# Performance work log

Hardware: AMD Instinct MI355X
Metric: run time of the kernel (lower is better)

The kernel has to match this reference:

```python
import jax, jax.numpy as jnp
import numpy as np

N = 100_000   # nodes
E = 1_600_000 # edges
IN, HID, OUT = 128, 64, 32


def _glorot(key, fan_in, fan_out):
    s = jnp.sqrt(6.0 / (fan_in + fan_out)).astype(jnp.float32)
    return jax.random.uniform(key, (fan_in, fan_out), jnp.float32, -s, s)


def setup_inputs() -> dict:
    key = jax.random.key(0)
    ks = jax.random.split(key, 8)
    x = jax.random.normal(ks[0], (N, IN), jnp.float32)
    edge_index = jax.random.randint(ks[1], (2, E), 0, N, jnp.int64)
    return {
        "x": x,
        "edge_index": edge_index,
        "W1": _glorot(ks[2], IN, HID),
        "b1": jnp.zeros((HID,), jnp.float32),
        "W_mu": _glorot(ks[3], HID, OUT),
        "b_mu": jnp.zeros((OUT,), jnp.float32),
        "W_ls": _glorot(ks[4], HID, OUT),
        "b_ls": jnp.zeros((OUT,), jnp.float32),
    }


def _gcn_conv(x, W, b, src, dst, n, dinv_sqrt):
    """PyG GCNConv: h = x @ W; symmetric-normalized scatter-add incl. self-loops; + b."""
    h = x @ W                                       # [N, F_out]
    coef = dinv_sqrt[src] * dinv_sqrt[dst]          # [E]
    msg = h[src] * coef[:, None]                    # [E, F_out] gather
    agg = jax.ops.segment_sum(msg, dst, num_segments=n)  # scatter-add
    agg = agg + h * (dinv_sqrt * dinv_sqrt)[:, None]      # self-loop contribution
    return agg + b


def reference(x, edge_index, W1, b1, W_mu, b_mu, W_ls, b_ls):
    src, dst = edge_index[0], edge_index[1]
    n = x.shape[0]
    # degree on graph with self-loops (edge weight 1), shared by all three convs
    deg = jax.ops.segment_sum(jnp.ones((src.shape[0],), x.dtype), dst, num_segments=n) + 1.0
    dinv_sqrt = jax.lax.rsqrt(deg)
    h = jax.nn.relu(_gcn_conv(x, W1, b1, src, dst, n, dinv_sqrt))
    mu = _gcn_conv(h, W_mu, b_mu, src, dst, n, dinv_sqrt)
    logstd = _gcn_conv(h, W_ls, b_ls, src, dst, n, dinv_sqrt)
    return mu, logstd
```

## Files before the change

### kernel.cpp

```cpp
#include <hip/hip_runtime.h>
#include <hip/hip_bf16.h>

#define FIN 128
#define HID 64
#define BSN 128
#define BSHIFT 7
#define SRCBITS 20
#define EPB 8192
#define BSTRIDE 2304
#define STARTBITS 21

typedef __attribute__((ext_vector_type(8))) short short8;
typedef __attribute__((ext_vector_type(4))) float floatx4;

__device__ __forceinline__ float bf2f(unsigned short u) {
    union { unsigned int i; float f; } c;
    c.i = ((unsigned int)u) << 16;
    return c.f;
}

__device__ __forceinline__ unsigned short f2bf(float f) {
    union { float f; unsigned int i; } c;
    c.f = f;
    unsigned int u = c.i;
    unsigned int r = (u + 0x7FFFu + ((u >> 16) & 1u)) >> 16;
    return (unsigned short)r;
}

__global__ void bin_fill(const int* __restrict__ src, const int* __restrict__ dst,
                         int* __restrict__ bcur, unsigned* __restrict__ rec, int E) {
    __shared__ int hist[1024];
    __shared__ int cbase[1024];
    for (int i = threadIdx.x; i < 1024; i += 256) hist[i] = 0;
    __syncthreads();
    int base = blockIdx.x * EPB;
    int lim = min(base + EPB, E);
    for (int e = base + threadIdx.x; e < lim; e += 256)
        atomicAdd(&hist[dst[e] >> BSHIFT], 1);
    __syncthreads();
    for (int b = threadIdx.x; b < 1024; b += 256) {
        int c = hist[b];
        cbase[b] = c ? atomicAdd(&bcur[b], c) : 0;
    }
    __syncthreads();
    for (int i = threadIdx.x; i < 1024; i += 256) hist[i] = 0;
    __syncthreads();
    for (int e = base + threadIdx.x; e < lim; e += 256) {
        int d = dst[e];
        int bkt = d >> BSHIFT;
        int slot = atomicAdd(&hist[bkt], 1);
        rec[bkt * BSTRIDE + cbase[bkt] + slot] =
            (unsigned)src[e] | ((unsigned)(d & (BSN - 1)) << SRCBITS);
    }
}

__global__ void csr_build(const unsigned* __restrict__ rec, const int* __restrict__ bcur,
                          unsigned* __restrict__ rowp, int* __restrict__ csr, int N) {
    __shared__ int cnt[BSN], excl[BSN], cur[BSN];
    int b = blockIdx.x, t = threadIdx.x;
    if (t < BSN) cnt[t] = 0;
    __syncthreads();
    int base = b * BSTRIDE;
    int cb = bcur[b];
    for (int i = t; i < cb; i += 256)
        atomicAdd(&cnt[rec[base + i] >> SRCBITS], 1);
    __syncthreads();
    if (t < BSN) excl[t] = cnt[t];
    __syncthreads();
    for (int off = 1; off < BSN; off <<= 1) {
        int a = 0;
        if (t < BSN && t >= off) a = excl[t - off];
        __syncthreads();
        if (t < BSN) excl[t] += a;
        __syncthreads();
    }
    if (t < BSN) {
        int inc = excl[t];
        int ex = inc - cnt[t];
        excl[t] = ex;
        cur[t] = 0;
        int n = b * BSN + t;
        if (n < N)
            rowp[n] = (unsigned)(base + ex) | ((unsigned)cnt[t] << STARTBITS);
    }
    __syncthreads();
    for (int i = t; i < cb; i += 256) {
        unsigned r = rec[base + i];
        int dl = r >> SRCBITS;
        int slot = atomicAdd(&cur[dl], 1);
        csr[base + excl[dl] + slot] = (int)(r & ((1u << SRCBITS) - 1));
    }
}

__global__ __launch_bounds__(256) void gemm1_mfma(
    const float* __restrict__ x, const float* __restrict__ W1,
    const unsigned* __restrict__ rowp, unsigned short* __restrict__ h0, int N) {
    __shared__ unsigned short Wt[64][136];
    {
        int t = threadIdx.x;
        int k  = t >> 1;
        int c0 = (t & 1) << 5;
        const float* wr = W1 + k * HID + c0;
#pragma unroll
        for (int cc = 0; cc < 32; ++cc)
            Wt[c0 + cc][k] = f2bf(wr[cc]);
    }
    __syncthreads();
    int wave = threadIdx.x >> 6, lane = threadIdx.x & 63;
    int m = lane & 15, q = lane >> 4;
    short8 bfr[4][4];
#pragma unroll
    for (int ct = 0; ct < 4; ++ct)
#pragma unroll
        for (int kk = 0; kk < 4; ++kk)
            bfr[ct][kk] = *((const short8*)&Wt[ct * 16 + m][kk * 32 + q * 8]);
    int ntiles = N >> 4;
    for (int t = blockIdx.x * 4 + wave; t < ntiles; t += gridDim.x * 4) {
        int nbase = t << 4;
        const float* xr = x + (size_t)(nbase + m) * FIN + q * 8;
        short8 afr[4];
#pragma unroll
        for (int kk = 0; kk < 4; ++kk) {
            float4 p0 = *((const float4*)(xr + kk * 32));
            float4 p1 = *((const float4*)(xr + kk * 32 + 4));
            short8 ta;
            ta[0] = (short)f2bf(p0.x); ta[1] = (short)f2bf(p0.y);
            ta[2] = (short)f2bf(p0.z); ta[3] = (short)f2bf(p0.w);
            ta[4] = (short)f2bf(p1.x); ta[5] = (short)f2bf(p1.y);
            ta[6] = (short)f2bf(p1.z); ta[7] = (short)f2bf(p1.w);
            afr[kk] = ta;
        }
        uint4 rp = *((const uint4*)(rowp + nbase + q * 4));
        floatx4 cacc[4];
#pragma unroll
        for (int ct = 0; ct < 4; ++ct) cacc[ct] = floatx4{0.f, 0.f, 0.f, 0.f};
#pragma unroll
        for (int ct = 0; ct < 4; ++ct)
#pragma unroll
            for (int kk = 0; kk < 4; ++kk)
                cacc[ct] = __builtin_amdgcn_mfma_f32_16x16x32_bf16(afr[kk], bfr[ct][kk], cacc[ct], 0, 0, 0);
#pragma unroll
        for (int ct = 0; ct < 4; ++ct) {
#pragma unroll
            for (int r = 0; r < 4; ++r) {
                unsigned pr = (r == 0) ? rp.x : (r == 1) ? rp.y : (r == 2) ? rp.z : rp.w;
                float d = rsqrtf((float)(pr >> STARTBITS) + 1.0f);
                int n = nbase + q * 4 + r;
                h0[(size_t)n * HID + ct * 16 + m] = f2bf(cacc[ct][r] * d);
            }
        }
    }
}


#define ACC8(a, d)                                                      \
    do {                                                                \
        union { unsigned u; float f; } c_;                              \
        c_.u = (d).x << 16;          a[0] += c_.f;                      \
        c_.u = (d).x & 0xFFFF0000u;  a[1] += c_.f;                      \
        c_.u = (d).y << 16;          a[2] += c_.f;                      \
        c_.u = (d).y & 0xFFFF0000u;  a[3] += c_.f;                      \
        c_.u = (d).z << 16;          a[4] += c_.f;                      \
        c_.u = (d).z & 0xFFFF0000u;  a[5] += c_.f;                      \
        c_.u = (d).w << 16;          a[6] += c_.f;                      \
        c_.u = (d).w & 0xFFFF0000u;  a[7] += c_.f;                      \
    } while (0)

template <int MODE>
__global__ __launch_bounds__(256, 4) void pull(
    const unsigned short* __restrict__ hp,
    const unsigned* __restrict__ rowp,
    const int* __restrict__ csr,
    const float* __restrict__ b1,
    unsigned short* __restrict__ outp,
    const float* __restrict__ Wmu, const float* __restrict__ bmu,
    const float* __restrict__ Wls, const float* __restrict__ bls,
    float* __restrict__ out, int N) {
    int lane = threadIdx.x & 63;
    int wave = threadIdx.x >> 6;
    int nd8  = lane >> 3;
    int g    = lane & 7;
    int n = blockIdx.x * 32 + wave * 8 + nd8;
    bool valid = (n < N);
    int nc = valid ? n : 0;
    unsigned rp = rowp[nc];
    int start = (int)(rp & ((1u << STARTBITS) - 1u));
    int deg   = (int)(rp >> STARTBITS);
    int end   = valid ? start + deg : 0;
    if (!valid) start = 0;
    const char* hpb = (const char*)hp;
    unsigned goff = (unsigned)(g << 4);
    uint4 sv = *((const uint4*)(hpb + (((unsigned)nc) << 7) + goff));
    float di = rsqrtf((float)deg + 1.0f);
    float4 bb0 = *((const float4*)(b1 + (g << 3)));
    float4 bb1 = *((const float4*)(b1 + (g << 3) + 4));
    float a[8] = {0.f, 0.f, 0.f, 0.f, 0.f, 0.f, 0.f, 0.f};
    int j = start;
    for (; j + 8 <= end; j += 8) {
        int s0 = csr[j],     s1 = csr[j + 1], s2 = csr[j + 2], s3 = csr[j + 3];
        int s4 = csr[j + 4], s5 = csr[j + 5], s6 = csr[j + 6], s7 = csr[j + 7];
        uint4 d0 = *((const uint4*)(hpb + (((unsigned)s0) << 7) + goff));
        uint4 d1 = *((const uint4*)(hpb + (((unsigned)s1) << 7) + goff));
        uint4 d2 = *((const uint4*)(hpb + (((unsigned)s2) << 7) + goff));
        uint4 d3 = *((const uint4*)(hpb + (((unsigned)s3) << 7) + goff));
        uint4 d4 = *((const uint4*)(hpb + (((unsigned)s4) << 7) + goff));
        uint4 d5 = *((const uint4*)(hpb + (((unsigned)s5) << 7) + goff));
        uint4 d6 = *((const uint4*)(hpb + (((unsigned)s6) << 7) + goff));
        uint4 d7 = *((const uint4*)(hpb + (((unsigned)s7) << 7) + goff));
        ACC8(a, d0); ACC8(a, d1); ACC8(a, d2); ACC8(a, d3);
        ACC8(a, d4); ACC8(a, d5); ACC8(a, d6); ACC8(a, d7);
    }
    if (j + 4 <= end) {
        int s0 = csr[j], s1 = csr[j + 1], s2 = csr[j + 2], s3 = csr[j + 3];
        uint4 d0 = *((const uint4*)(hpb + (((unsigned)s0) << 7) + goff));
        uint4 d1 = *((const uint4*)(hpb + (((unsigned)s1) << 7) + goff));
        uint4 d2 = *((const uint4*)(hpb + (((unsigned)s2) << 7) + goff));
        uint4 d3 = *((const uint4*)(hpb + (((unsigned)s3) << 7) + goff));
        ACC8(a, d0); ACC8(a, d1); ACC8(a, d2); ACC8(a, d3);
        j += 4;
    }
    if (j < end) {
        int i0 = j, i1 = min(j + 1, end - 1), i2 = min(j + 2, end - 1);
        int s0 = csr[i0], s1 = csr[i1], s2 = csr[i2];
        uint4 d0 = *((const uint4*)(hpb + (((unsigned)s0) << 7) + goff));
        uint4 d1 = *((const uint4*)(hpb + (((unsigned)s1) << 7) + goff));
        uint4 d2 = *((const uint4*)(hpb + (((unsigned)s2) << 7) + goff));
        if (j + 1 >= end) { d1.x = 0u; d1.y = 0u; d1.z = 0u; d1.w = 0u; }
        if (j + 2 >= end) { d2.x = 0u; d2.y = 0u; d2.z = 0u; d2.w = 0u; }
        ACC8(a, d0); ACC8(a, d1); ACC8(a, d2);
    }
    uint4 o = {0u, 0u, 0u, 0u};
    if (valid) {
        ACC8(a, sv);
        float v[8];
        if (MODE == 0) {
            float t0;
            t0 = di * a[0] + bb0.x; v[0] = (t0 > 0.f ? t0 : 0.f) * di;
            t0 = di * a[1] + bb0.y; v[1] = (t0 > 0.f ? t0 : 0.f) * di;
            t0 = di * a[2] + bb0.z; v[2] = (t0 > 0.f ? t0 : 0.f) * di;
            t0 = di * a[3] + bb0.w; v[3] = (t0 > 0.f ? t0 : 0.f) * di;
            t0 = di * a[4] + bb1.x; v[4] = (t0 > 0.f ? t0 : 0.f) * di;
            t0 = di * a[5] + bb1.y; v[5] = (t0 > 0.f ? t0 : 0.f) * di;
            t0 = di * a[6] + bb1.z; v[6] = (t0 > 0.f ? t0 : 0.f) * di;
            t0 = di * a[7] + bb1.w; v[7] = (t0 > 0.f ? t0 : 0.f) * di;
        } else {
#pragma unroll
            for (int k = 0; k < 8; ++k) v[k] = di * a[k];
        }
        o.x = (unsigned)f2bf(v[0]) | ((unsigned)f2bf(v[1]) << 16);
        o.y = (unsigned)f2bf(v[2]) | ((unsigned)f2bf(v[3]) << 16);
        o.z = (unsigned)f2bf(v[4]) | ((unsigned)f2bf(v[5]) << 16);
        o.w = (unsigned)f2bf(v[6]) | ((unsigned)f2bf(v[7]) << 16);
    }
    if constexpr (MODE == 0) {
        if (valid)
            *((uint4*)(outp + (size_t)n * HID + (g << 3))) = o;
    } else {
        __shared__ unsigned short ab[32][68];
        *((uint4*)&ab[wave * 8 + nd8][g << 3]) = o;
        __syncthreads();
        int m = lane & 15, q = lane >> 4;
        int tileId = wave >> 1;
        int ct0 = (wave & 1) * 2;
        short8 a0 = *((const short8*)&ab[tileId * 16 + m][q * 8]);
        short8 a1 = *((const short8*)&ab[tileId * 16 + m][32 + q * 8]);
        short8 bfr[2][2];
        float bias[2];
#pragma unroll
        for (int c = 0; c < 2; ++c) {
            int col = (ct0 + c) * 16 + m;
#pragma unroll
            for (int kk = 0; kk < 2; ++kk) {
                short8 tf;
#pragma unroll
                for (int jj = 0; jj < 8; ++jj) {
                    int k = kk * 32 + q * 8 + jj;
                    float w = (col < 32) ? Wmu[k * 32 + col] : Wls[k * 32 + (col - 32)];
                    tf[jj] = (short)f2bf(w);
                }
                bfr[c][kk] = tf;
            }
            bias[c] = (col < 32) ? bmu[col] : bls[col - 32];
        }
        floatx4 cc[2];
#pragma unroll
        for (int c = 0; c < 2; ++c) cc[c] = floatx4{0.f, 0.f, 0.f, 0.f};
#pragma unroll
        for (int c = 0; c < 2; ++c) {
            cc[c] = __builtin_amdgcn_mfma_f32_16x16x32_bf16(a0, bfr[c][0], cc[c], 0, 0, 0);
            cc[c] = __builtin_amdgcn_mfma_f32_16x16x32_bf16(a1, bfr[c][1], cc[c], 0, 0, 0);
        }
        int nb = blockIdx.x * 32 + tileId * 16;
#pragma unroll
        for (int c = 0; c < 2; ++c) {
            int col = (ct0 + c) * 16 + m;
            int which = col >> 5, oc = col & 31;
#pragma unroll
            for (int r = 0; r < 4; ++r) {
                int n2 = nb + q * 4 + r;
                if (n2 < N)
                    out[(size_t)which * N * 32 + (size_t)n2 * 32 + oc] = cc[c][r] + bias[c];
            }
        }
    }
}

extern "C" void kernel_launch(void* const* d_in, const int* in_sizes, int n_in,
                              void* d_out, int out_size, void* d_ws, size_t ws_size,
                              hipStream_t stream) {
    const float* x   = (const float*)d_in[0];
    const int*   ei  = (const int*)d_in[1];
    const float* W1  = (const float*)d_in[2];
    const float* b1  = (const float*)d_in[3];
    const float* Wmu = (const float*)d_in[4];
    const float* bmu = (const float*)d_in[5];
    const float* Wls = (const float*)d_in[6];
    const float* bls = (const float*)d_in[7];
    int N = in_sizes[0] / FIN;
    int E = in_sizes[1] / 2;
    const int* src = ei;
    const int* dst = ei + E;
    float* out = (float*)d_out;

    int B = (N + BSN - 1) / BSN;
    int nbin = (E + EPB - 1) / EPB;

    unsigned* rowp = (unsigned*)d_ws;
    int* bcur = (int*)(rowp + N);
    int* csr  = bcur + B;
    unsigned short* bufA = (unsigned short*)(csr + (size_t)B * BSTRIDE);
    char* region2 = (char*)(bufA + (size_t)N * HID);
    unsigned* rec        = (unsigned*)region2;
    unsigned short* bufB = (unsigned short*)region2;

    hipMemsetAsync(bcur, 0, (size_t)B * sizeof(int), stream);
    bin_fill<<<nbin, 256, 0, stream>>>(src, dst, bcur, rec, E);
    csr_build<<<B, 256, 0, stream>>>(rec, bcur, rowp, csr, N);

    gemm1_mfma<<<512, 256, 0, stream>>>(x, W1, rowp, bufA, N);

    int pgrid = (N + 31) / 32;
    pull<0><<<pgrid, 256, 0, stream>>>(bufA, rowp, csr, b1, bufB,
                                       Wmu, bmu, Wls, bls, out, N);
    pull<1><<<pgrid, 256, 0, stream>>>(bufB, rowp, csr, b1, (unsigned short*)0,
                                       Wmu, bmu, Wls, bls, out, N);
}
```

Before: 260.9 us.

## Replace shared-memory histogram binning with direct padded global atomics

The binning kernel drops its two-pass per-block shared histogram and reservation scheme. Each edge now does a global atomicAdd on a per-bucket counter, padded to 16 ints so counters sit on separate cache lines, and writes its record straight into the bucket. The grid becomes a fixed 2048-block grid-stride loop. This removes the extra pass over dst and the block barriers, at the cost of one global atomic per edge (1.6M) with contention spread over about 782 buckets.

```diff
diff --git a/kernel.cpp b/kernel.cpp
--- a/kernel.cpp
+++ b/kernel.cpp
@@ -6,9 +6,9 @@
 #define BSN 128
 #define BSHIFT 7
 #define SRCBITS 20
-#define EPB 8192
 #define BSTRIDE 2304
 #define STARTBITS 21
+#define BPAD 16
 
 typedef __attribute__((ext_vector_type(8))) short short8;
 typedef __attribute__((ext_vector_type(4))) float floatx4;
@@ -27,30 +27,18 @@
     return (unsigned short)r;
 }
 
-__global__ void bin_fill(const int* __restrict__ src, const int* __restrict__ dst,
-                         int* __restrict__ bcur, unsigned* __restrict__ rec, int E) {
-    __shared__ int hist[1024];
-    __shared__ int cbase[1024];
-    for (int i = threadIdx.x; i < 1024; i += 256) hist[i] = 0;
-    __syncthreads();
-    int base = blockIdx.x * EPB;
-    int lim = min(base + EPB, E);
-    for (int e = base + threadIdx.x; e < lim; e += 256)
-        atomicAdd(&hist[dst[e] >> BSHIFT], 1);
-    __syncthreads();
-    for (int b = threadIdx.x; b < 1024; b += 256) {
-        int c = hist[b];
-        cbase[b] = c ? atomicAdd(&bcur[b], c) : 0;
-    }
-    __syncthreads();
-    for (int i = threadIdx.x; i < 1024; i += 256) hist[i] = 0;
-    __syncthreads();
-    for (int e = base + threadIdx.x; e < lim; e += 256) {
+__global__ __launch_bounds__(256) void bin_fill(
+    const int* __restrict__ src, const int* __restrict__ dst,
+    int* __restrict__ bcur, unsigned* __restrict__ rec, int E) {
+    int i = blockIdx.x * 256 + threadIdx.x;
+    int stride = gridDim.x * 256;
+    for (int e = i; e < E; e += stride) {
         int d = dst[e];
+        int s = src[e];
         int bkt = d >> BSHIFT;
-        int slot = atomicAdd(&hist[bkt], 1);
-        rec[bkt * BSTRIDE + cbase[bkt] + slot] =
-            (unsigned)src[e] | ((unsigned)(d & (BSN - 1)) << SRCBITS);
+        int slot = atomicAdd(&bcur[bkt * BPAD], 1);
+        rec[bkt * BSTRIDE + slot] =
+            (unsigned)s | ((unsigned)(d & (BSN - 1)) << SRCBITS);
     }
 }
 
@@ -61,7 +49,7 @@
     if (t < BSN) cnt[t] = 0;
     __syncthreads();
     int base = b * BSTRIDE;
-    int cb = bcur[b];
+    int cb = bcur[b * BPAD];
     for (int i = t; i < cb; i += 256)
         atomicAdd(&cnt[rec[base + i] >> SRCBITS], 1);
     __syncthreads();
@@ -323,17 +311,17 @@
     float* out = (float*)d_out;
 
     int B = (N + BSN - 1) / BSN;
-    int nbin = (E + EPB - 1) / EPB;
 
     unsigned* rowp = (unsigned*)d_ws;
     int* bcur = (int*)(rowp + N);
-    int* csr  = bcur + B;
+    int* csr  = bcur + (size_t)B * BPAD;
     unsigned short* bufA = (unsigned short*)(csr + (size_t)B * BSTRIDE);
     char* region2 = (char*)(bufA + (size_t)N * HID);
     unsigned* rec        = (unsigned*)region2;
     unsigned short* bufB = (unsigned short*)region2;
 
-    hipMemsetAsync(bcur, 0, (size_t)B * sizeof(int), stream);
+    hipMemsetAsync(bcur, 0, (size_t)B * BPAD * sizeof(int), stream);
+    int nbin = 2048;
     bin_fill<<<nbin, 256, 0, stream>>>(src, dst, bcur, rec, E);
     csr_build<<<B, 256, 0, stream>>>(rec, bcur, rowp, csr, N);
 
```

Result: slower. 279.2 us (+7.0%).
